# Kernel optimization log

Measured on AMD Instinct MI355X. Metric: run time of the kernel, lower is better.

The kernel has to match this reference:

```python
import jax, jax.numpy as jnp
import numpy as np

BS, C, H, W = 64, 2048, 14, 14
D = 768            # decoder_embedding
G = 100            # embed_len_decoder (groups)
F = 10             # duplicate_factor = ceil(1000/100)
NUM_CLASSES = 1000
HEADS, DH = 8, 768 # dim_head = decoder_embedding
INNER = HEADS * DH # 6144
FF = 2048          # dim_feedforward


def setup_inputs() -> dict:
    key = jax.random.key(0)
    ks = jax.random.split(key, 26)
    s = 0.02
    return {
        "x": jax.random.normal(ks[0], (BS, C, H, W), jnp.float32),
        "W_embed": jax.random.normal(ks[1], (C, D), jnp.float32) * s,
        "b_embed": jnp.zeros((D,), jnp.float32),
        "query_embed": jax.random.normal(ks[2], (G, D), jnp.float32),
        "ln1_g": jnp.ones((D,), jnp.float32), "ln1_b": jnp.zeros((D,), jnp.float32),
        "Wq_s": jax.random.normal(ks[3], (D, INNER), jnp.float32) * s,
        "Wk_s": jax.random.normal(ks[4], (D, INNER), jnp.float32) * s,
        "Wv_s": jax.random.normal(ks[5], (D, INNER), jnp.float32) * s,
        "Wo_s": jax.random.normal(ks[6], (INNER, D), jnp.float32) * s,
        "bo_s": jnp.zeros((D,), jnp.float32),
        "ln2_g": jnp.ones((D,), jnp.float32), "ln2_b": jnp.zeros((D,), jnp.float32),
        "Wq_c": jax.random.normal(ks[7], (D, INNER), jnp.float32) * s,
        "Wk_c": jax.random.normal(ks[8], (D, INNER), jnp.float32) * s,
        "Wv_c": jax.random.normal(ks[9], (D, INNER), jnp.float32) * s,
        "Wo_c": jax.random.normal(ks[10], (INNER, D), jnp.float32) * s,
        "bo_c": jnp.zeros((D,), jnp.float32),
        "ln3_g": jnp.ones((D,), jnp.float32), "ln3_b": jnp.zeros((D,), jnp.float32),
        "W1": jax.random.normal(ks[11], (D, FF), jnp.float32) * s,
        "b1": jnp.zeros((FF,), jnp.float32),
        "W2": jax.random.normal(ks[12], (FF, D), jnp.float32) * s,
        "b2": jnp.zeros((D,), jnp.float32),
        "dup_pool": jax.random.normal(ks[13], (G, D, F), jnp.float32) * s,
        "dup_bias": jnp.zeros((NUM_CLASSES,), jnp.float32),
    }


def _ln(x, g, b, eps=1e-5):
    mu = jnp.mean(x, -1, keepdims=True)
    var = jnp.mean(jnp.square(x - mu), -1, keepdims=True)
    return g * (x - mu) * jax.lax.rsqrt(var + eps) + b


def _attn(q_in, kv_in, Wq, Wk, Wv, Wo, bo):
    b, nq, _ = q_in.shape
    nk = kv_in.shape[1]
    q = (q_in @ Wq).reshape(b, nq, HEADS, DH).transpose(0, 2, 1, 3)
    k = (kv_in @ Wk).reshape(b, nk, HEADS, DH).transpose(0, 2, 1, 3)
    v = (kv_in @ Wv).reshape(b, nk, HEADS, DH).transpose(0, 2, 1, 3)
    scores = jnp.einsum("bhqd,bhkd->bhqk", q, k) * (DH ** -0.5)
    a = jax.nn.softmax(scores, axis=-1)
    o = jnp.einsum("bhqk,bhkd->bhqd", a, v).transpose(0, 2, 1, 3).reshape(b, nq, INNER)
    return o @ Wo + bo


def reference(x, W_embed, b_embed, query_embed,
              ln1_g, ln1_b, Wq_s, Wk_s, Wv_s, Wo_s, bo_s,
              ln2_g, ln2_b, Wq_c, Wk_c, Wv_c, Wo_c, bo_c,
              ln3_g, ln3_b, W1, b1, W2, b2,
              dup_pool, dup_bias):
    bs = x.shape[0]
    # [bs, C, H, W] -> [bs, H*W, C] spatial tokens
    emb = x.reshape(bs, x.shape[1], -1).transpose(0, 2, 1)
    emb = jax.nn.relu(emb @ W_embed + b_embed)          # [bs, HW, D]
    h = jnp.broadcast_to(query_embed[None], (bs, G, D))  # query tokens
    # one pre-norm decoder layer: self-attn, cross-attn, GELU MLP
    hn = _ln(h, ln1_g, ln1_b)
    h = h + _attn(hn, hn, Wq_s, Wk_s, Wv_s, Wo_s, bo_s)
    h = h + _attn(_ln(h, ln2_g, ln2_b), emb, Wq_c, Wk_c, Wv_c, Wo_c, bo_c)
    hn = _ln(h, ln3_g, ln3_b)
    h = h + (jax.nn.gelu(hn @ W1 + b1) @ W2 + b2)
    # GroupFC: per-group matmul -> single batched einsum
    out_extrap = jnp.einsum("bgd,gdf->bgf", h, dup_pool)  # [bs, G, F]
    logits = out_extrap.reshape(bs, G * F)[:, :NUM_CLASSES] + dup_bias
    return logits
```

## Files before the change

kernel.cpp:

```cpp
#include <hip/hip_runtime.h>
#include <hip/hip_bf16.h>


typedef __attribute__((ext_vector_type(8))) short short8;
typedef __attribute__((ext_vector_type(4))) short short4b;
typedef __attribute__((ext_vector_type(4))) float floatx4;

#define DEVI static __device__ __forceinline__

DEVI short f2bf(float f) {
    union { __hip_bfloat16 h; short s; } u;
    u.h = __float2bfloat16(f);
    return u.s;
}

DEVI float bf2f(short s) {
    union { float f; unsigned u; } v;
    v.u = ((unsigned)(unsigned short)s) << 16;
    return v.f;
}

DEVI void gld_lds16(const void* g, void* l) {
    __builtin_amdgcn_global_load_lds(
        (const __attribute__((address_space(1))) void*)g,
        (__attribute__((address_space(3))) void*)l, 16, 0, 0);
}

__global__ __launch_bounds__(256)
void prep_kernel(const float* __restrict__ W_embed, const float* __restrict__ W1,
                 const float* __restrict__ W2, const float* __restrict__ Wq_s,
                 const float* __restrict__ Wk_s, const float* __restrict__ Wv_s,
                 const float* __restrict__ Wo_s, const float* __restrict__ Wo_c,
                 const float* __restrict__ Wq_c, const float* __restrict__ Wk_c,
                 const float* __restrict__ Wv_c, const float* __restrict__ x,
                 const float* __restrict__ qe, const float* __restrict__ ln1_g,
                 const float* __restrict__ ln1_b,
                 short* __restrict__ WembT, short* __restrict__ W1T,
                 short* __restrict__ W2T, short* __restrict__ WqsT,
                 short* __restrict__ WksT, short* __restrict__ WvsT,
                 short* __restrict__ WosT, short* __restrict__ WoTc,
                 short* __restrict__ CQ, short* __restrict__ CK,
                 short* __restrict__ CV, short* __restrict__ xT,
                 short* __restrict__ hn1)
{
    const int bid = blockIdx.x;
    const int t = threadIdx.x;

    if (bid >= 6912 && bid < 20736) {
        int lb = bid - 6912;
        const float* in; short* out;
        if (lb < 4608)       { in = Wq_c; out = CQ; }
        else if (lb < 9216)  { in = Wk_c; out = CK; lb -= 4608; }
        else                 { in = Wv_c; out = CV; lb -= 9216; }
        const long i = (long)lb * 256 + t;
        const float4 v = ((const float4*)in)[i];
        short4b s; s[0] = f2bf(v.x); s[1] = f2bf(v.y); s[2] = f2bf(v.z); s[3] = f2bf(v.w);
        ((short4b*)out)[i] = s;
        return;
    }

    __shared__ __align__(16) short tile[64][65];

    if (bid >= 28928) {
        const int row = bid - 28928;
        float* ss  = (float*)&tile[0][0];
        float* ssq = ss + 4;
        float4 v = {0.f, 0.f, 0.f, 0.f};
        float s = 0.f, sq = 0.f;
        if (t < 192) {
            v = *(const float4*)(qe + (long)row * 768 + (t << 2));
            s  = v.x + v.y + v.z + v.w;
            sq = v.x * v.x + v.y * v.y + v.z * v.z + v.w * v.w;
            #pragma unroll
            for (int off = 32; off; off >>= 1) {
                s  += __shfl_xor(s, off);
                sq += __shfl_xor(sq, off);
            }
            if ((t & 63) == 0) { ss[t >> 6] = s; ssq[t >> 6] = sq; }
        }
        __syncthreads();
        if (t < 192) {
            s  = ss[0] + ss[1] + ss[2];
            sq = ssq[0] + ssq[1] + ssq[2];
            const float mean = s * (1.0f / 768.0f);
            const float var  = sq * (1.0f / 768.0f) - mean * mean;
            const float rstd = rsqrtf(var + 1e-5f);
            const float4 gv = *(const float4*)(ln1_g + (t << 2));
            const float4 bv = *(const float4*)(ln1_b + (t << 2));
            short4b o;
            o[0] = f2bf((v.x - mean) * rstd * gv.x + bv.x);
            o[1] = f2bf((v.y - mean) * rstd * gv.y + bv.y);
            o[2] = f2bf((v.z - mean) * rstd * gv.z + bv.z);
            o[3] = f2bf((v.w - mean) * rstd * gv.w + bv.w);
            *(short4b*)(hn1 + (long)row * 768 + (t << 2)) = o;
        }
        return;
    }

    const float* in; short* out; int R, C, ldo, bx, by;
    long ioff = 0, ooff = 0;
    if (bid < 384)       { in = W_embed; out = WembT; R = 2048; C = 768;  ldo = 2048; bx = bid % 12;  by = bid / 12; }
    else if (bid < 768)  { const int l = bid - 384;  in = W1;   out = W1T;  R = 768;  C = 2048; ldo = 768;  bx = l % 32; by = l / 32; }
    else if (bid < 1152) { const int l = bid - 768;  in = W2;   out = W2T;  R = 2048; C = 768;  ldo = 2048; bx = l % 12; by = l / 12; }
    else if (bid < 2304) { const int l = bid - 1152; in = Wq_s; out = WqsT; R = 768;  C = 6144; ldo = 768;  bx = l % 96; by = l / 96; }
    else if (bid < 3456) { const int l = bid - 2304; in = Wk_s; out = WksT; R = 768;  C = 6144; ldo = 768;  bx = l % 96; by = l / 96; }
    else if (bid < 4608) { const int l = bid - 3456; in = Wv_s; out = WvsT; R = 768;  C = 6144; ldo = 768;  bx = l % 96; by = l / 96; }
    else if (bid < 5760) { const int l = bid - 4608; in = Wo_s; out = WosT; R = 6144; C = 768;  ldo = 6144; bx = l % 12; by = l / 12; }
    else if (bid < 6912) { const int l = bid - 5760; in = Wo_c; out = WoTc; R = 6144; C = 768;  ldo = 6144; bx = l % 12; by = l / 12; }
    else {
        const int l = bid - 20736;
        const int z = l >> 7, rem = l & 127;
        in = x; out = xT; R = 2048; C = 196; ldo = 2048;
        bx = rem % 4; by = rem / 4;
        ioff = (long)z * 2048 * 196;
        ooff = (long)z * 196 * 2048;
    }

    const int bxo = bx << 6, byo = by << 6;
    const int tx = t & 63, ty = t >> 6;
    #pragma unroll
    for (int i = ty; i < 64; i += 4) {
        const int r = byo + i, c = bxo + tx;
        short v = 0;
        if (r < R && c < C) v = f2bf(in[ioff + (long)r * C + c]);
        tile[i][tx] = v;
    }
    __syncthreads();
    #pragma unroll
    for (int i = ty; i < 64; i += 4) {
        const int c = bxo + i, r = byo + tx;
        if (c < C && r < ldo) out[ooff + (long)c * ldo + r] = tile[tx][i];
    }
}

template<int ACT, bool OUT_BF16, int TBM>
__global__ __launch_bounds__(256)
void gemm_kernel(const short* __restrict__ Ap, const short* __restrict__ Bp,
                 const float* __restrict__ bias, const float* __restrict__ resid,
                 int rmod, void* __restrict__ Cp,
                 int M, int N, int K, int Mpad, int Npad,
                 int lda, int ldb, int ldc, int inner_batch,
                 long sA1, long sA2, long sB1, long sB2, long sC1, long sC2,
                 float alpha)
{
    constexpr int BK_ = 64;
    constexpr int MI  = TBM / 32;
    constexpr int ATS = TBM * BK_;
    constexpr int BTS = 128 * BK_;
    __shared__ __align__(16) short lds_all[2 * (ATS + BTS)];

    const int gx = gridDim.x, gy = gridDim.y;
    const long nwg = (long)gx * gy * gridDim.z;
    const long dfl = blockIdx.x + (long)gx * (blockIdx.y + (long)gy * blockIdx.z);
    const long qch = nwg >> 3, rch = nwg & 7;
    const long xcd = dfl & 7, idx = dfl >> 3;
    const long w = (xcd < rch ? xcd * (qch + 1) : rch * (qch + 1) + (xcd - rch) * qch) + idx;
    const int bx = (int)(w % gx);
    const long wt = w / gx;
    const int by = (int)(wt % gy);
    const int bz = (int)(wt / gy);

    const int outer = bz / inner_batch;
    const int inner = bz - outer * inner_batch;
    const long aoff = (long)outer * sA1 + (long)inner * sA2;
    const long boff = (long)outer * sB1 + (long)inner * sB2;
    const long coff = (long)outer * sC1 + (long)inner * sC2;
    const int m0 = by * TBM, n0 = bx * 128;
    const int tid = threadIdx.x;
    const int wid = tid >> 6, lane = tid & 63;
    const int wm = (wid >> 1) * (TBM / 2);
    const int wn = (wid & 1) << 6;
    const int fr = lane & 15;
    const int fk = (lane >> 4) << 3;

    const short* A = Ap + aoff;
    const short* B = Bp + boff;
    const int rowp = tid >> 3;
    const int col8 = (tid & 7) << 3;
    const int wrow = (tid >> 6) << 3;

    const bool fastA0 = (m0 + TBM <= Mpad);
    const bool fastB0 = (n0 + 128 <= Npad);

    auto stage = [&](int buf, int kt) {
        short (*As)[BK_] = reinterpret_cast<short (*)[BK_]>(lds_all + buf * (ATS + BTS));
        short (*Bs)[BK_] = reinterpret_cast<short (*)[BK_]>(lds_all + buf * (ATS + BTS) + ATS);
        if (fastA0 && (kt + BK_ <= K)) {
            const short* src = A + (long)(m0 + rowp) * lda + kt + col8;
            const long rstride = (long)lda << 5;
            #pragma unroll
            for (int p = 0; p < TBM / 32; ++p)
                gld_lds16(src + p * rstride, &As[(p << 5) + wrow][0]);
        } else {
            #pragma unroll
            for (int i = 0; i < TBM / 32; ++i) {
                const int row = rowp + (i << 5);
                const int gm = m0 + row, gk = kt + col8;
                short8 v;
                if (gm < M && gk + 8 <= K) {
                    v = *(const short8*)(A + (long)gm * lda + gk);
                } else {
                    #pragma unroll
                    for (int j = 0; j < 8; ++j)
                        v[j] = (gm < M && gk + j < K) ? A[(long)gm * lda + gk + j] : (short)0;
                }
                *(short8*)(&As[row][col8]) = v;
            }
        }
        if (fastB0 && (kt + BK_ <= K)) {
            const short* src = B + (long)(n0 + rowp) * ldb + kt + col8;
            const long rstride = (long)ldb << 5;
            #pragma unroll
            for (int p = 0; p < 4; ++p)
                gld_lds16(src + p * rstride, &Bs[(p << 5) + wrow][0]);
        } else {
            #pragma unroll
            for (int i = 0; i < 4; ++i) {
                const int row = rowp + (i << 5);
                const int gn = n0 + row, gk = kt + col8;
                short8 v;
                if (gn < N && gk + 8 <= K) {
                    v = *(const short8*)(B + (long)gn * ldb + gk);
                } else {
                    #pragma unroll
                    for (int j = 0; j < 8; ++j)
                        v[j] = (gn < N && gk + j < K) ? B[(long)gn * ldb + gk + j] : (short)0;
                }
                *(short8*)(&Bs[row][col8]) = v;
            }
        }
    };

    floatx4 acc[MI][4] = {};
    const int nk = K / BK_;

    stage(0, 0);
    __syncthreads();
    for (int t = 0; t < nk; ++t) {
        const int cur = t & 1;
        if (t + 1 < nk) stage(cur ^ 1, (t + 1) * BK_);
        const short* As = lds_all + cur * (ATS + BTS);
        const short* Bs = lds_all + cur * (ATS + BTS) + ATS;
        #pragma unroll
        for (int kk = 0; kk < BK_; kk += 32) {
            short8 af[MI], bfv[4];
            #pragma unroll
            for (int i = 0; i < MI; ++i)
                af[i] = *(const short8*)(As + (wm + (i << 4) + fr) * BK_ + kk + fk);
            #pragma unroll
            for (int j = 0; j < 4; ++j)
                bfv[j] = *(const short8*)(Bs + (wn + (j << 4) + fr) * BK_ + kk + fk);
            #pragma unroll
            for (int i = 0; i < MI; ++i)
                #pragma unroll
                for (int j = 0; j < 4; ++j)
                    acc[i][j] = __builtin_amdgcn_mfma_f32_16x16x32_bf16(af[i], bfv[j], acc[i][j], 0, 0, 0);
        }
        __syncthreads();
    }

    if constexpr (OUT_BF16) {
        short (*Cl)[128] = reinterpret_cast<short (*)[128]>(lds_all);
        #pragma unroll
        for (int j = 0; j < 4; ++j) {
            const int lcol = wn + (j << 4) + fr;
            const float bv = bias ? bias[n0 + lcol] : 0.0f;
            #pragma unroll
            for (int i = 0; i < MI; ++i) {
                #pragma unroll
                for (int r = 0; r < 4; ++r) {
                    const int lrow = wm + (i << 4) + ((lane >> 4) << 2) + r;
                    float v = acc[i][j][r] * alpha + bv;
                    if constexpr (ACT == 1) v = fmaxf(v, 0.0f);
                    if constexpr (ACT == 2) {
                        v = 0.5f * v * (1.0f + tanhf(0.7978845608028654f * (v + 0.044715f * v * v * v)));
                    }
                    if (resid)
                        v += resid[(long)((m0 + lrow) % rmod) * ldc + n0 + lcol];
                    Cl[lrow][lcol] = f2bf(v);
                }
            }
        }
        __syncthreads();
        const int pr = tid >> 4;
        const int pc = (tid & 15) << 3;
        #pragma unroll
        for (int it = 0; it < TBM / 16; ++it) {
            const int row = (it << 4) + pr;
            const int gm = m0 + row;
            if (gm < M)
                *(short8*)((short*)Cp + coff + (long)gm * ldc + n0 + pc) =
                    *(const short8*)(&Cl[row][pc]);
        }
    } else {
        #pragma unroll
        for (int j = 0; j < 4; ++j) {
            const int col = n0 + wn + (j << 4) + fr;
            if (col >= N) continue;
            const float bv = bias ? bias[col] : 0.0f;
            #pragma unroll
            for (int i = 0; i < MI; ++i) {
                #pragma unroll
                for (int r = 0; r < 4; ++r) {
                    const int row = m0 + wm + (i << 4) + ((lane >> 4) << 2) + r;
                    if (row >= M) continue;
                    float v = acc[i][j][r] * alpha + bv;
                    if constexpr (ACT == 1) v = fmaxf(v, 0.0f);
                    if constexpr (ACT == 2) {
                        v = 0.5f * v * (1.0f + tanhf(0.7978845608028654f * (v + 0.044715f * v * v * v)));
                    }
                    const long ci = coff + (long)row * ldc + col;
                    if (resid) v += resid[(long)(row % rmod) * ldc + col];
                    ((float*)Cp)[ci] = v;
                }
            }
        }
    }
}

template<int NTT, int RI>
__global__ __launch_bounds__(256)
void attn_kernel(const short* __restrict__ Qp, const short* __restrict__ Kp,
                 const short* __restrict__ VTp, short* __restrict__ Cp,
                 int nt, int nh,
                 int ldq, int ldk, int ldv, int ldc,
                 int khs, int vhs,
                 long sK, long sVT, long sC,
                 float scale)
{
    constexpr int KP   = NTT * 16;
    constexpr int PLD  = KP + 8;
    constexpr int ROWS = RI * 64;
    constexpr int KS_SH = KP * 64;
    constexpr int P_SH  = ROWS * PLD;
    constexpr int LDS_SH = (KS_SH > P_SH) ? KS_SH : P_SH;
    __shared__ __align__(16) short lds[LDS_SH];
    short (*Pl)[PLD] = reinterpret_cast<short (*)[PLD]>(lds);

    const int blk = blockIdx.x;
    const int nb = gridDim.x / nh;
    int b, h;
    if (nb == 64) {
        b = ((blk & 7) << 3) + (blk >> 6);
        h = (blk >> 3) & 7;
    } else {
        b = blk / nh; h = blk - b * nh;
    }
    const int row0 = blockIdx.z * ROWS;

    const int tid = threadIdx.x, wid = tid >> 6, lane = tid & 63;
    const int fr = lane & 15;
    const int g4 = (lane >> 4) << 2;
    const int fk = (lane >> 4) << 3;

    const short* Qh = Qp + h * 768;
    const short* Kb = Kp + (long)b * sK + h * khs;
    const short* Vb = VTp + (long)b * sVT + (long)h * vhs * ldv;

    const int wmA = wid * (RI * 16);
    floatx4 accS[RI][NTT];
    #pragma unroll
    for (int i = 0; i < RI; ++i)
        #pragma unroll
        for (int j = 0; j < NTT; ++j) accS[i][j] = (floatx4){0.f, 0.f, 0.f, 0.f};

    const short* qrow[RI];
    #pragma unroll
    for (int i = 0; i < RI; ++i)
        qrow[i] = Qh + (long)(row0 + wmA + i * 16 + fr) * ldq + fk;

    const int rowg  = (wid << 3) + (lane >> 3);
    const int slotx = ((lane & 7) ^ ((lane >> 3) & 7)) << 3;
    const short* ksrc = Kb + (long)rowg * ldk + slotx;
    short* kdst0 = lds + (wid << 9);

    for (int t = 0; t < 12; ++t) {
        const int kt = t << 6;
        #pragma unroll
        for (int p = 0; p < KP / 32; ++p)
            gld_lds16(ksrc + ((long)(p << 5) * ldk + kt), kdst0 + (p << 11));
        __syncthreads();
        #pragma unroll
        for (int kkb = 0; kkb < 2; ++kkb) {
            const int kk = kkb << 5;
            short8 aF[RI];
            #pragma unroll
            for (int i = 0; i < RI; ++i)
                aF[i] = *(const short8*)(qrow[i] + kt + kk);
            const int sl = ((((kk >> 3) + (lane >> 4)) ^ (fr & 7)) << 3);
            #pragma unroll
            for (int j = 0; j < NTT; ++j) {
                const short8 bF = *(const short8*)(lds + ((j << 4) + fr) * 64 + sl);
                #pragma unroll
                for (int i = 0; i < RI; ++i)
                    accS[i][j] = __builtin_amdgcn_mfma_f32_16x16x32_bf16(aF[i], bF, accS[i][j], 0, 0, 0);
            }
        }
        __syncthreads();
    }

    float inv[RI][4];
    #pragma unroll
    for (int i = 0; i < RI; ++i) {
        #pragma unroll
        for (int r = 0; r < 4; ++r) {
            float m = -1e30f;
            #pragma unroll
            for (int j = 0; j < NTT; ++j) {
                const int col = j * 16 + fr;
                if (col < nt) m = fmaxf(m, accS[i][j][r]);
            }
            #pragma unroll
            for (int off = 1; off < 16; off <<= 1) m = fmaxf(m, __shfl_xor(m, off));
            float s = 0.0f;
            #pragma unroll
            for (int j = 0; j < NTT; ++j) {
                const int col = j * 16 + fr;
                float e = (col < nt) ? __expf((accS[i][j][r] - m) * scale) : 0.0f;
                accS[i][j][r] = e;
                s += e;
            }
            #pragma unroll
            for (int off = 1; off < 16; off <<= 1) s += __shfl_xor(s, off);
            inv[i][r] = 1.0f / s;
        }
    }

    #pragma unroll
    for (int i = 0; i < RI; ++i)
        #pragma unroll
        for (int j = 0; j < NTT; ++j)
            #pragma unroll
            for (int r = 0; r < 4; ++r)
                Pl[wmA + i * 16 + g4 + r][j * 16 + fr] = f2bf(accS[i][j][r] * inv[i][r]);
    __syncthreads();

    constexpr int WGN = (RI == 2) ? 2 : 4;
    constexpr int NSTEP = WGN * 64;
    const int wm2 = (wid / WGN) << 6;
    const int wn2 = (wid % WGN) << 6;
    short* Cb = Cp + (long)b * sC + h * 768;

    const int chunk = 768 / gridDim.y;
    const int n0b = blockIdx.y * chunk;
    for (int n0 = n0b; n0 < n0b + chunk; n0 += NSTEP) {
        floatx4 acc2[4][4];
        #pragma unroll
        for (int i = 0; i < 4; ++i)
            #pragma unroll
            for (int j = 0; j < 4; ++j) acc2[i][j] = (floatx4){0.f, 0.f, 0.f, 0.f};
        #pragma unroll
        for (int kk = 0; kk < KP; kk += 32) {
            short8 aF[4], bF[4];
            #pragma unroll
            for (int i = 0; i < 4; ++i)
                aF[i] = *(const short8*)(&Pl[wm2 + i * 16 + fr][kk + fk]);
            #pragma unroll
            for (int j = 0; j < 4; ++j)
                bF[j] = *(const short8*)(Vb + (long)(n0 + wn2 + j * 16 + fr) * ldv + kk + fk);
            #pragma unroll
            for (int i = 0; i < 4; ++i)
                #pragma unroll
                for (int j = 0; j < 4; ++j)
                    acc2[i][j] = __builtin_amdgcn_mfma_f32_16x16x32_bf16(aF[i], bF[j], acc2[i][j], 0, 0, 0);
        }
        #pragma unroll
        for (int j = 0; j < 4; ++j) {
            const int col = n0 + wn2 + (j << 4) + fr;
            #pragma unroll
            for (int i = 0; i < 4; ++i) {
                #pragma unroll
                for (int r = 0; r < 4; ++r) {
                    const int row = row0 + wm2 + (i << 4) + g4 + r;
                    if (row < 100)
                        Cb[(long)row * ldc + col] = f2bf(acc2[i][j][r]);
                }
            }
        }
    }
}

template<int NTT>
__global__ __launch_bounds__(512)
void attn8_kernel(const short* __restrict__ Qp, const short* __restrict__ Kp,
                  const short* __restrict__ VTp, short* __restrict__ Cp,
                  int nt, int ldq, int ldk, int ldv, int ldc,
                  long sK, long sVT, long sC, float scale)
{
    constexpr int KP   = NTT * 16;
    constexpr int PLD  = KP + 8;
    constexpr int KBUF = KP * 64;
    constexpr int P_SH = 128 * PLD;
    constexpr int LDS_SH = (2 * KBUF > P_SH) ? 2 * KBUF : P_SH;
    __shared__ __align__(16) short lds[LDS_SH];
    short (*Pl)[PLD] = reinterpret_cast<short (*)[PLD]>(lds);

    const int blk = blockIdx.x;
    const int b = ((blk & 7) << 3) + (blk >> 6);
    const int h = (blk >> 3) & 7;

    const int tid = threadIdx.x, wid = tid >> 6, lane = tid & 63;
    const int fr = lane & 15;
    const int g4 = (lane >> 4) << 2;
    const int fk = (lane >> 4) << 3;

    const short* Qh = Qp + h * 768;
    const short* Kb = Kp + (long)b * sK;
    const short* Vb = VTp + (long)b * sVT;

    const int wmA = wid << 4;
    floatx4 accS[NTT];
    #pragma unroll
    for (int j = 0; j < NTT; ++j) accS[j] = (floatx4){0.f, 0.f, 0.f, 0.f};

    const short* qrow = Qh + (long)(wmA + fr) * ldq + fk;

    const int rowg  = (wid << 3) + (lane >> 3);
    const int slotx = ((lane & 7) ^ ((lane >> 3) & 7)) << 3;
    const short* ksrc = Kb + (long)rowg * ldk + slotx;

    auto stageK = [&](int buf, int kt) {
        short* dst = lds + buf * KBUF + (wid << 9);
        #pragma unroll
        for (int p = 0; p < 4; ++p)
            if (p < 3 || wid < 4)
                gld_lds16(ksrc + ((long)(p << 6) * ldk + kt), dst + (p << 12));
    };

    stageK(0, 0);
    __syncthreads();
    for (int t = 0; t < 12; ++t) {
        const int cur = t & 1;
        if (t < 11) stageK(cur ^ 1, (t + 1) << 6);
        const int kt = t << 6;
        const short* kb = lds + cur * KBUF;
        #pragma unroll
        for (int kkb = 0; kkb < 2; ++kkb) {
            const int kk = kkb << 5;
            const short8 aF = *(const short8*)(qrow + kt + kk);
            const int sl = ((((kk >> 3) + (lane >> 4)) ^ (fr & 7)) << 3);
            #pragma unroll
            for (int j = 0; j < NTT; ++j) {
                const short8 bF = *(const short8*)(kb + ((j << 4) + fr) * 64 + sl);
                accS[j] = __builtin_amdgcn_mfma_f32_16x16x32_bf16(aF, bF, accS[j], 0, 0, 0);
            }
        }
        __syncthreads();
    }

    float inv_[4];
    #pragma unroll
    for (int r = 0; r < 4; ++r) {
        float m = -1e30f;
        #pragma unroll
        for (int j = 0; j < NTT; ++j) {
            const int col = j * 16 + fr;
            if (col < nt) m = fmaxf(m, accS[j][r]);
        }
        #pragma unroll
        for (int off = 1; off < 16; off <<= 1) m = fmaxf(m, __shfl_xor(m, off));
        float s = 0.0f;
        #pragma unroll
        for (int j = 0; j < NTT; ++j) {
            const int col = j * 16 + fr;
            float e = (col < nt) ? __expf((accS[j][r] - m) * scale) : 0.0f;
            accS[j][r] = e;
            s += e;
        }
        #pragma unroll
        for (int off = 1; off < 16; off <<= 1) s += __shfl_xor(s, off);
        inv_[r] = 1.0f / s;
    }

    #pragma unroll
    for (int j = 0; j < NTT; ++j)
        #pragma unroll
        for (int r = 0; r < 4; ++r)
            Pl[wmA + g4 + r][j * 16 + fr] = f2bf(accS[j][r] * inv_[r]);
    __syncthreads();

    const int wm2 = (wid >> 2) << 6;
    const int wn2 = (wid & 3) << 6;
    short* Cb = Cp + (long)b * sC + h * 768;

    for (int n0 = 0; n0 < 768; n0 += 256) {
        #pragma unroll
        for (int jh = 0; jh < 2; ++jh) {
            floatx4 acc2[4][2];
            #pragma unroll
            for (int i = 0; i < 4; ++i)
                #pragma unroll
                for (int j = 0; j < 2; ++j) acc2[i][j] = (floatx4){0.f, 0.f, 0.f, 0.f};
            #pragma unroll
            for (int kk = 0; kk < KP; kk += 32) {
                short8 aF[4], bF[2];
                #pragma unroll
                for (int i = 0; i < 4; ++i)
                    aF[i] = *(const short8*)(&Pl[wm2 + i * 16 + fr][kk + fk]);
                #pragma unroll
                for (int j = 0; j < 2; ++j)
                    bF[j] = *(const short8*)(Vb + (long)(n0 + wn2 + (jh * 2 + j) * 16 + fr) * ldv + kk + fk);
                #pragma unroll
                for (int i = 0; i < 4; ++i)
                    #pragma unroll
                    for (int j = 0; j < 2; ++j)
                        acc2[i][j] = __builtin_amdgcn_mfma_f32_16x16x32_bf16(aF[i], bF[j], acc2[i][j], 0, 0, 0);
            }
            #pragma unroll
            for (int j = 0; j < 2; ++j) {
                const int col = n0 + wn2 + ((jh * 2 + j) << 4) + fr;
                #pragma unroll
                for (int i = 0; i < 4; ++i) {
                    #pragma unroll
                    for (int r = 0; r < 4; ++r) {
                        const int row = wm2 + (i << 4) + g4 + r;
                        if (row < 100)
                            Cb[(long)row * ldc + col] = f2bf(acc2[i][j][r]);
                    }
                }
            }
        }
    }
}

template<bool IN_F32>
__global__ __launch_bounds__(256)
void transpose_kernel(const void* __restrict__ inp, short* __restrict__ outp,
                      int R, int Cc, int ldout)
{
    __shared__ short tile[64][65];
    const long in_off = (long)blockIdx.z * R * Cc;
    const long out_off = (long)blockIdx.z * Cc * ldout;
    const int bx = blockIdx.x << 6;
    const int by = blockIdx.y << 6;
    const int tx = threadIdx.x & 63, ty = threadIdx.x >> 6;
    #pragma unroll
    for (int i = ty; i < 64; i += 4) {
        const int r = by + i, c = bx + tx;
        short v = 0;
        if (r < R && c < Cc) {
            if constexpr (IN_F32) v = f2bf(((const float*)inp)[in_off + (long)r * Cc + c]);
            else                  v = ((const short*)inp)[in_off + (long)r * Cc + c];
        }
        tile[i][tx] = v;
    }
    __syncthreads();
    #pragma unroll
    for (int i = ty; i < 64; i += 4) {
        const int c = bx + i, r = by + tx;
        if (c < Cc && r < ldout) outp[out_off + (long)c * ldout + r] = tile[tx][i];
    }
}

__global__ __launch_bounds__(192)
void ln_kernel(const float* __restrict__ x, const float* __restrict__ g,
               const float* __restrict__ b, short* __restrict__ out)
{
    const long row = blockIdx.x;
    const float* xr = x + row * 768;
    const int t = threadIdx.x;
    const float4 v = *(const float4*)(xr + (t << 2));
    float s  = v.x + v.y + v.z + v.w;
    float sq = v.x * v.x + v.y * v.y + v.z * v.z + v.w * v.w;
    #pragma unroll
    for (int off = 32; off; off >>= 1) {
        s  += __shfl_xor(s, off);
        sq += __shfl_xor(sq, off);
    }
    __shared__ float ss[4], ssq[4];
    const int w = t >> 6;
    if ((t & 63) == 0) { ss[w] = s; ssq[w] = sq; }
    __syncthreads();
    s  = ss[0] + ss[1] + ss[2];
    sq = ssq[0] + ssq[1] + ssq[2];
    const float mean = s * (1.0f / 768.0f);
    const float var  = sq * (1.0f / 768.0f) - mean * mean;
    const float rstd = rsqrtf(var + 1e-5f);
    const float4 gv = *(const float4*)(g + (t << 2));
    const float4 bv = *(const float4*)(b + (t << 2));
    short4b o;
    o[0] = f2bf((v.x - mean) * rstd * gv.x + bv.x);
    o[1] = f2bf((v.y - mean) * rstd * gv.y + bv.y);
    o[2] = f2bf((v.z - mean) * rstd * gv.z + bv.z);
    o[3] = f2bf((v.w - mean) * rstd * gv.w + bv.w);
    *(short4b*)(out + row * 768 + (t << 2)) = o;
}

template<bool DO_LN, bool PBF16>
__global__ __launch_bounds__(192)
void reduce_kernel(const void* __restrict__ part, int nsplit, long pstride,
                   const float* __restrict__ resid, int rmod,
                   const float* __restrict__ bias,
                   const float* __restrict__ g, const float* __restrict__ bvec,
                   float* __restrict__ hout, short* __restrict__ hnout)
{
    const long row = blockIdx.x;
    const int t = threadIdx.x;
    const int c = t << 2;
    const float* rr = resid + (long)(row % rmod) * 768;
    float4 v = *(const float4*)(rr + c);
    const float4 bb = *(const float4*)(bias + c);
    v.x += bb.x; v.y += bb.y; v.z += bb.z; v.w += bb.w;
    for (int s = 0; s < nsplit; ++s) {
        const long idx = (long)s * pstride + row * 768 + c;
        if constexpr (PBF16) {
            const short4b p = *(const short4b*)((const short*)part + idx);
            v.x += bf2f(p[0]); v.y += bf2f(p[1]); v.z += bf2f(p[2]); v.w += bf2f(p[3]);
        } else {
            const float4 p = *(const float4*)((const float*)part + idx);
            v.x += p.x; v.y += p.y; v.z += p.z; v.w += p.w;
        }
    }
    *(float4*)(hout + row * 768 + c) = v;
    if constexpr (DO_LN) {
        float s  = v.x + v.y + v.z + v.w;
        float sq = v.x * v.x + v.y * v.y + v.z * v.z + v.w * v.w;
        #pragma unroll
        for (int off = 32; off; off >>= 1) {
            s  += __shfl_xor(s, off);
            sq += __shfl_xor(sq, off);
        }
        __shared__ float ss[4], ssq[4];
        const int wv = t >> 6;
        if ((t & 63) == 0) { ss[wv] = s; ssq[wv] = sq; }
        __syncthreads();
        s  = ss[0] + ss[1] + ss[2];
        sq = ssq[0] + ssq[1] + ssq[2];
        const float mean = s * (1.0f / 768.0f);
        const float var  = sq * (1.0f / 768.0f) - mean * mean;
        const float rstd = rsqrtf(var + 1e-5f);
        const float4 gv = *(const float4*)(g + c);
        const float4 bv = *(const float4*)(bvec + c);
        short4b o;
        o[0] = f2bf((v.x - mean) * rstd * gv.x + bv.x);
        o[1] = f2bf((v.y - mean) * rstd * gv.y + bv.y);
        o[2] = f2bf((v.z - mean) * rstd * gv.z + bv.z);
        o[3] = f2bf((v.w - mean) * rstd * gv.w + bv.w);
        *(short4b*)(hnout + row * 768 + c) = o;
    }
}

__global__ __launch_bounds__(192)
void reducen_kernel(const short* __restrict__ part, int nsplit, long pstride,
                    short* __restrict__ out, int grps)
{
    const int blk = blockIdx.x;
    const int row = blk / grps, grp = blk - row * grps;
    const long base = (long)row * grps * 768 + grp * 768 + (threadIdx.x << 2);
    float4 v = {0.f, 0.f, 0.f, 0.f};
    for (int s = 0; s < nsplit; ++s) {
        const short4b p = *(const short4b*)(part + (long)s * pstride + base);
        v.x += bf2f(p[0]); v.y += bf2f(p[1]); v.z += bf2f(p[2]); v.w += bf2f(p[3]);
    }
    short4b o;
    o[0] = f2bf(v.x); o[1] = f2bf(v.y); o[2] = f2bf(v.z); o[3] = f2bf(v.w);
    *(short4b*)(out + base) = o;
}

__global__ __launch_bounds__(64)
void groupfc_kernel(const float* __restrict__ h, const float* __restrict__ dp,
                    const float* __restrict__ bias, float* __restrict__ out)
{
    const int bg = blockIdx.x;
    const int g = bg % 100;
    const int t = threadIdx.x;
    const float* hr = h + (long)bg * 768;
    const float* d = dp + (long)g * 7680;
    float acc[10];
    #pragma unroll
    for (int f = 0; f < 10; ++f) acc[f] = 0.0f;
    for (int k = t; k < 768; k += 64) {
        const float hv = hr[k];
        const float* dr = d + k * 10;
        #pragma unroll
        for (int f = 0; f < 10; ++f) acc[f] += hv * dr[f];
    }
    #pragma unroll
    for (int f = 0; f < 10; ++f) {
        #pragma unroll
        for (int off = 32; off; off >>= 1) acc[f] += __shfl_xor(acc[f], off);
    }
    if (t == 0) {
        const int b = bg / 100;
        #pragma unroll
        for (int f = 0; f < 10; ++f)
            out[(long)b * 1000 + g * 10 + f] = acc[f] + bias[g * 10 + f];
    }
}

extern "C" void kernel_launch(void* const* d_in, const int* in_sizes, int n_in,
                              void* d_out, int out_size, void* d_ws, size_t ws_size,
                              hipStream_t stream)
{
    const float* x       = (const float*)d_in[0];
    const float* W_embed = (const float*)d_in[1];
    const float* b_embed = (const float*)d_in[2];
    const float* qe      = (const float*)d_in[3];
    const float* ln1_g   = (const float*)d_in[4];
    const float* ln1_b   = (const float*)d_in[5];
    const float* Wq_s    = (const float*)d_in[6];
    const float* Wk_s    = (const float*)d_in[7];
    const float* Wv_s    = (const float*)d_in[8];
    const float* Wo_s    = (const float*)d_in[9];
    const float* bo_s    = (const float*)d_in[10];
    const float* ln2_g   = (const float*)d_in[11];
    const float* ln2_b   = (const float*)d_in[12];
    const float* Wq_c    = (const float*)d_in[13];
    const float* Wk_c    = (const float*)d_in[14];
    const float* Wv_c    = (const float*)d_in[15];
    const float* Wo_c    = (const float*)d_in[16];
    const float* bo_c    = (const float*)d_in[17];
    const float* ln3_g   = (const float*)d_in[18];
    const float* ln3_b   = (const float*)d_in[19];
    const float* W1      = (const float*)d_in[20];
    const float* b1      = (const float*)d_in[21];
    const float* W2      = (const float*)d_in[22];
    const float* b2      = (const float*)d_in[23];
    const float* dpool   = (const float*)d_in[24];
    const float* dbias   = (const float*)d_in[25];

    char* base = (char*)d_ws;
    size_t off = 0;
    auto alloc = [&](size_t bytes) -> void* {
        void* p = base + off;
        off += (bytes + 255) & ~(size_t)255;
        return p;
    };
    short* ek    = (short*)alloc(12544L * 768 * 2);
    short* ekT   = (short*)alloc(64L * 768 * 256 * 2);
    short* big   = (short*)alloc(6400L * 6144 * 2);
    char*  shr   = (char*) alloc(4L * 6400 * 768 * 4);
    float* h2    = (float*)alloc(6400L * 768 * 4);
    short* hn3   = (short*)alloc(6400L * 768 * 2);
    short* t1    = (short*)alloc(6400L * 2048 * 2);
    short* WembT = (short*)alloc(768L * 2048 * 2);
    short* W1T   = (short*)alloc(2048L * 768 * 2);
    short* W2T   = (short*)alloc(768L * 2048 * 2);
    short* WqkTc = (short*)alloc(6144L * 768 * 2);
    short* WvoTc = (short*)alloc(768L * 6144 * 2);
    short* WqsT  = (short*)alloc(6144L * 768 * 2);
    short* WksT  = (short*)alloc(6144L * 768 * 2);
    short* WvsT  = (short*)alloc(6144L * 768 * 2);
    short* WosT  = (short*)alloc(768L * 6144 * 2);
    short* hn1   = (short*)alloc(128L * 768 * 2);
    short* q_s   = (short*)alloc(128L * 6144 * 2);
    short* k_s   = (short*)alloc(128L * 6144 * 2);
    short* v_s   = (short*)alloc(128L * 6144 * 2);
    short* ctx_s = (short*)alloc(128L * 6144 * 2);
    short* v_sT  = (short*)alloc(6144L * 128 * 2);
    short* qt_c  = (short*)alloc(128L * 6144 * 2);
    short* qtP   = (short*)alloc(4L * 100 * 6144 * 2);
    float* partS = (float*)alloc(8L * 100 * 768 * 4);
    float* h1    = (float*)alloc(128L * 768 * 4);
    short* hn2   = (short*)alloc(128L * 768 * 2);
    (void)ws_size; (void)in_sizes; (void)n_in; (void)out_size;

    short* CQ    = (short*)shr;
    short* CK    = CQ + 4718592L;
    short* CV    = CK + 4718592L;
    short* WoTc  = CV + 4718592L;
    short* partCb = (short*)shr;

    const float scale = 0.03608439182435161f;

    short* xT = big;
    prep_kernel<<<dim3(29028), 256, 0, stream>>>(
        W_embed, W1, W2, Wq_s, Wk_s, Wv_s, Wo_s, Wo_c,
        Wq_c, Wk_c, Wv_c, x, qe, ln1_g, ln1_b,
        WembT, W1T, W2T, WqsT, WksT, WvsT, WosT, WoTc,
        CQ, CK, CV, xT, hn1);

    gemm_kernel<0, true, 128><<<dim3(6, 6, 8), 256, 0, stream>>>(
        CK, CQ, nullptr, nullptr, 1, WqkTc,
        768, 768, 768, 768, 768, 6144, 6144, 768, 8,
        0L, 768L, 0L, 768L, 0L, 589824L, 1.0f);
    gemm_kernel<0, true, 128><<<dim3(6, 6, 8), 256, 0, stream>>>(
        WoTc, CV, nullptr, nullptr, 1, WvoTc,
        768, 768, 768, 768, 768, 6144, 6144, 6144, 8,
        0L, 768L, 0L, 768L, 0L, 768L, 1.0f);

    gemm_kernel<1, true, 64><<<dim3(6, 196, 1), 256, 0, stream>>>(
        xT, WembT, b_embed, nullptr, 1, ek,
        12544, 768, 2048, 12544, 768, 2048, 2048, 768, 1,
        0L, 0L, 0L, 0L, 0L, 0L, 1.0f);
    transpose_kernel<false><<<dim3(12, 4, 64), 256, 0, stream>>>(ek, ekT, 196, 768, 256);

    gemm_kernel<0, true, 128><<<dim3(48, 1, 3), 256, 0, stream>>>(
        hn1, WqsT, nullptr, nullptr, 1, q_s,
        100, 6144, 768, 128, 6144, 768, 768, 6144, 1,
        0L, 0L, 4718592L, 0L, 786432L, 0L, 1.0f);
    transpose_kernel<false><<<dim3(96, 2, 1), 256, 0, stream>>>(v_s, v_sT, 100, 6144, 128);
    attn_kernel<8, 2><<<dim3(8, 6, 1), 256, 0, stream>>>(
        q_s, k_s, v_sT, ctx_s,
        100, 8, 6144, 6144, 128, 6144,
        768, 768, 0L, 0L, 0L, scale);
    gemm_kernel<0, false, 128><<<dim3(6, 1, 8), 256, 0, stream>>>(
        ctx_s, WosT, nullptr, nullptr, 1, partS,
        100, 768, 768, 128, 768, 6144, 6144, 768, 8,
        0L, 768L, 0L, 768L, 0L, 76800L, 1.0f);
    reduce_kernel<true, false><<<dim3(100), 192, 0, stream>>>(
        partS, 8, 76800L, qe, 100, bo_s, ln2_g, ln2_b, h1, hn2);

    gemm_kernel<0, true, 128><<<dim3(48, 1, 4), 256, 0, stream>>>(
        hn2, WqkTc, nullptr, nullptr, 1, qtP,
        100, 6144, 192, 128, 6144, 768, 768, 6144, 4,
        0L, 192L, 0L, 192L, 0L, 614400L, 1.0f);
    reducen_kernel<<<dim3(800), 192, 0, stream>>>(qtP, 4, 614400L, qt_c, 8);
    attn8_kernel<14><<<dim3(512), 512, 0, stream>>>(
        qt_c, ek, ekT, big,
        196, 6144, 768, 256, 6144,
        150528L, 196608L, 614400L, scale);
    gemm_kernel<0, true, 128><<<dim3(6, 50, 8), 256, 0, stream>>>(
        big, WvoTc, nullptr, nullptr, 1, partCb,
        6400, 768, 768, 6400, 768, 6144, 6144, 768, 8,
        0L, 768L, 0L, 768L, 0L, 4915200L, 1.0f);
    reduce_kernel<true, true><<<dim3(6400), 192, 0, stream>>>(
        partCb, 8, 4915200L, h1, 100, bo_c, ln3_g, ln3_b, h2, hn3);

    gemm_kernel<2, true, 64><<<dim3(16, 100, 1), 256, 0, stream>>>(
        hn3, W1T, b1, nullptr, 1, t1,
        6400, 2048, 768, 6400, 2048, 768, 768, 2048, 1, 0,0,0,0,0,0, 1.0f);
    gemm_kernel<0, true, 128><<<dim3(6, 50, 4), 256, 0, stream>>>(
        t1, W2T, nullptr, nullptr, 1, partCb,
        6400, 768, 512, 6400, 768, 2048, 2048, 768, 4,
        0L, 512L, 0L, 512L, 0L, 4915200L, 1.0f);
    reduce_kernel<false, true><<<dim3(6400), 192, 0, stream>>>(
        partCb, 4, 4915200L, h2, 6400, b2, nullptr, nullptr, h2, nullptr);

    groupfc_kernel<<<dim3(6400), 64, 0, stream>>>(h2, dpool, dbias, (float*)d_out);
}
```

Before: 752.2 us.

## Fuse fp32-to-bf16 weight conversion into GEMM operand loads, drop prep passes

Removes the separate prep passes that converted and transposed the self-attention weights and the cross-attention Q/K/V weights into bf16 scratch copies. The GEMMs now read fp32 weights directly and convert them to bf16 while staging into LDS. A new B mode transposes row-major weights into padded LDS, and an A mode does the same conversion for fp32 A operands. This saves the extra global write and re-read of about 100MB of weight copies. In exchange, the converting loads skip the direct global-to-LDS path and read fp32, which doubles the bytes loaded per GEMM tile, and the transposed LDS stores are scalar and may cause bank conflicts.

```diff
diff --git a/kernel.cpp b/kernel.cpp
--- a/kernel.cpp
+++ b/kernel.cpp
@@ -28,41 +28,21 @@
 
 __global__ __launch_bounds__(256)
 void prep_kernel(const float* __restrict__ W_embed, const float* __restrict__ W1,
-                 const float* __restrict__ W2, const float* __restrict__ Wq_s,
-                 const float* __restrict__ Wk_s, const float* __restrict__ Wv_s,
-                 const float* __restrict__ Wo_s, const float* __restrict__ Wo_c,
-                 const float* __restrict__ Wq_c, const float* __restrict__ Wk_c,
-                 const float* __restrict__ Wv_c, const float* __restrict__ x,
+                 const float* __restrict__ W2, const float* __restrict__ Wo_c,
+                 const float* __restrict__ x,
                  const float* __restrict__ qe, const float* __restrict__ ln1_g,
                  const float* __restrict__ ln1_b,
                  short* __restrict__ WembT, short* __restrict__ W1T,
-                 short* __restrict__ W2T, short* __restrict__ WqsT,
-                 short* __restrict__ WksT, short* __restrict__ WvsT,
-                 short* __restrict__ WosT, short* __restrict__ WoTc,
-                 short* __restrict__ CQ, short* __restrict__ CK,
-                 short* __restrict__ CV, short* __restrict__ xT,
-                 short* __restrict__ hn1)
+                 short* __restrict__ W2T, short* __restrict__ WoTc,
+                 short* __restrict__ xT, short* __restrict__ hn1)
 {
     const int bid = blockIdx.x;
     const int t = threadIdx.x;
 
-    if (bid >= 6912 && bid < 20736) {
-        int lb = bid - 6912;
-        const float* in; short* out;
-        if (lb < 4608)       { in = Wq_c; out = CQ; }
-        else if (lb < 9216)  { in = Wk_c; out = CK; lb -= 4608; }
-        else                 { in = Wv_c; out = CV; lb -= 9216; }
-        const long i = (long)lb * 256 + t;
-        const float4 v = ((const float4*)in)[i];
-        short4b s; s[0] = f2bf(v.x); s[1] = f2bf(v.y); s[2] = f2bf(v.z); s[3] = f2bf(v.w);
-        ((short4b*)out)[i] = s;
-        return;
-    }
-
     __shared__ __align__(16) short tile[64][65];
 
-    if (bid >= 28928) {
-        const int row = bid - 28928;
+    if (bid >= 10496) {
+        const int row = bid - 10496;
         float* ss  = (float*)&tile[0][0];
         float* ssq = ss + 4;
         float4 v = {0.f, 0.f, 0.f, 0.f};
@@ -102,13 +82,9 @@
     if (bid < 384)       { in = W_embed; out = WembT; R = 2048; C = 768;  ldo = 2048; bx = bid % 12;  by = bid / 12; }
     else if (bid < 768)  { const int l = bid - 384;  in = W1;   out = W1T;  R = 768;  C = 2048; ldo = 768;  bx = l % 32; by = l / 32; }
     else if (bid < 1152) { const int l = bid - 768;  in = W2;   out = W2T;  R = 2048; C = 768;  ldo = 2048; bx = l % 12; by = l / 12; }
-    else if (bid < 2304) { const int l = bid - 1152; in = Wq_s; out = WqsT; R = 768;  C = 6144; ldo = 768;  bx = l % 96; by = l / 96; }
-    else if (bid < 3456) { const int l = bid - 2304; in = Wk_s; out = WksT; R = 768;  C = 6144; ldo = 768;  bx = l % 96; by = l / 96; }
-    else if (bid < 4608) { const int l = bid - 3456; in = Wv_s; out = WvsT; R = 768;  C = 6144; ldo = 768;  bx = l % 96; by = l / 96; }
-    else if (bid < 5760) { const int l = bid - 4608; in = Wo_s; out = WosT; R = 6144; C = 768;  ldo = 6144; bx = l % 12; by = l / 12; }
-    else if (bid < 6912) { const int l = bid - 5760; in = Wo_c; out = WoTc; R = 6144; C = 768;  ldo = 6144; bx = l % 12; by = l / 12; }
+    else if (bid < 2304) { const int l = bid - 1152; in = Wo_c; out = WoTc; R = 6144; C = 768;  ldo = 6144; bx = l % 12; by = l / 12; }
     else {
-        const int l = bid - 20736;
+        const int l = bid - 2304;
         const int z = l >> 7, rem = l & 127;
         in = x; out = xT; R = 2048; C = 196; ldo = 2048;
         bx = rem % 4; by = rem / 4;
@@ -133,9 +109,9 @@
     }
 }
 
-template<int ACT, bool OUT_BF16, int TBM>
+template<int ACT, bool OUT_BF16, int TBM, int AM = 0, int BMODE = 0>
 __global__ __launch_bounds__(256)
-void gemm_kernel(const short* __restrict__ Ap, const short* __restrict__ Bp,
+void gemm_kernel(const void* __restrict__ Ap, const void* __restrict__ Bp,
                  const float* __restrict__ bias, const float* __restrict__ resid,
                  int rmod, void* __restrict__ Cp,
                  int M, int N, int K, int Mpad, int Npad,
@@ -145,8 +121,9 @@
 {
     constexpr int BK_ = 64;
     constexpr int MI  = TBM / 32;
+    constexpr int BLD = (BMODE == 2) ? 66 : 64;
     constexpr int ATS = TBM * BK_;
-    constexpr int BTS = 128 * BK_;
+    constexpr int BTS = 128 * BLD;
     __shared__ __align__(16) short lds_all[2 * (ATS + BTS)];
 
     const int gx = gridDim.x, gy = gridDim.y;
@@ -173,8 +150,6 @@
     const int fr = lane & 15;
     const int fk = (lane >> 4) << 3;
 
-    const short* A = Ap + aoff;
-    const short* B = Bp + boff;
     const int rowp = tid >> 3;
     const int col8 = (tid & 7) << 3;
     const int wrow = (tid >> 6) << 3;
@@ -183,50 +158,92 @@
     const bool fastB0 = (n0 + 128 <= Npad);
 
     auto stage = [&](int buf, int kt) {
-        short (*As)[BK_] = reinterpret_cast<short (*)[BK_]>(lds_all + buf * (ATS + BTS));
-        short (*Bs)[BK_] = reinterpret_cast<short (*)[BK_]>(lds_all + buf * (ATS + BTS) + ATS);
-        if (fastA0 && (kt + BK_ <= K)) {
-            const short* src = A + (long)(m0 + rowp) * lda + kt + col8;
-            const long rstride = (long)lda << 5;
-            #pragma unroll
-            for (int p = 0; p < TBM / 32; ++p)
-                gld_lds16(src + p * rstride, &As[(p << 5) + wrow][0]);
+        short* As = lds_all + buf * (ATS + BTS);
+        short* Bs = As + ATS;
+        if constexpr (AM == 0) {
+            const short* A = (const short*)Ap + aoff;
+            if (fastA0 && (kt + BK_ <= K)) {
+                const short* src = A + (long)(m0 + rowp) * lda + kt + col8;
+                const long rstride = (long)lda << 5;
+                #pragma unroll
+                for (int p = 0; p < TBM / 32; ++p)
+                    gld_lds16(src + p * rstride, As + ((p << 5) + wrow) * BK_);
+            } else {
+                #pragma unroll
+                for (int i = 0; i < TBM / 32; ++i) {
+                    const int row = rowp + (i << 5);
+                    const int gm = m0 + row, gk = kt + col8;
+                    short8 v;
+                    if (gm < M && gk + 8 <= K) {
+                        v = *(const short8*)(A + (long)gm * lda + gk);
+                    } else {
+                        #pragma unroll
+                        for (int j = 0; j < 8; ++j)
+                            v[j] = (gm < M && gk + j < K) ? A[(long)gm * lda + gk + j] : (short)0;
+                    }
+                    *(short8*)(As + row * BK_ + col8) = v;
+                }
+            }
         } else {
-            #pragma unroll
-            for (int i = 0; i < TBM / 32; ++i) {
-                const int row = rowp + (i << 5);
-                const int gm = m0 + row, gk = kt + col8;
-                short8 v;
-                if (gm < M && gk + 8 <= K) {
-                    v = *(const short8*)(A + (long)gm * lda + gk);
-                } else {
-                    #pragma unroll
-                    for (int j = 0; j < 8; ++j)
-                        v[j] = (gm < M && gk + j < K) ? A[(long)gm * lda + gk + j] : (short)0;
+            const float* A = (const float*)Ap + aoff;
+            const int r0 = tid >> 4, c4 = (tid & 15) << 2;
+            #pragma unroll
+            for (int i = 0; i < TBM / 16; ++i) {
+                const int row = r0 + (i << 4);
+                const int gm = m0 + row, gk = kt + c4;
+                float4 v = {0.f, 0.f, 0.f, 0.f};
+                if (gm < M) v = *(const float4*)(A + (long)gm * lda + gk);
+                short4b s; s[0] = f2bf(v.x); s[1] = f2bf(v.y); s[2] = f2bf(v.z); s[3] = f2bf(v.w);
+                *(short4b*)(As + row * BK_ + c4) = s;
+            }
+        }
+        if constexpr (BMODE == 0) {
+            const short* B = (const short*)Bp + boff;
+            if (fastB0 && (kt + BK_ <= K)) {
+                const short* src = B + (long)(n0 + rowp) * ldb + kt + col8;
+                const long rstride = (long)ldb << 5;
+                #pragma unroll
+                for (int p = 0; p < 4; ++p)
+                    gld_lds16(src + p * rstride, Bs + ((p << 5) + wrow) * BLD);
+            } else {
+                #pragma unroll
+                for (int i = 0; i < 4; ++i) {
+                    const int row = rowp + (i << 5);
+                    const int gn = n0 + row, gk = kt + col8;
+                    short8 v;
+                    if (gn < N && gk + 8 <= K) {
+                        v = *(const short8*)(B + (long)gn * ldb + gk);
+                    } else {
+                        #pragma unroll
+                        for (int j = 0; j < 8; ++j)
+                            v[j] = (gn < N && gk + j < K) ? B[(long)gn * ldb + gk + j] : (short)0;
+                    }
+                    *(short8*)(Bs + row * BLD + col8) = v;
                 }
-                *(short8*)(&As[row][col8]) = v;
-            }
-        }
-        if (fastB0 && (kt + BK_ <= K)) {
-            const short* src = B + (long)(n0 + rowp) * ldb + kt + col8;
-            const long rstride = (long)ldb << 5;
-            #pragma unroll
-            for (int p = 0; p < 4; ++p)
-                gld_lds16(src + p * rstride, &Bs[(p << 5) + wrow][0]);
+            }
+        } else if constexpr (BMODE == 1) {
+            const float* B = (const float*)Bp + boff;
+            const int r0 = tid >> 4, c4 = (tid & 15) << 2;
+            #pragma unroll
+            for (int i = 0; i < 8; ++i) {
+                const int row = r0 + (i << 4);
+                const int gn = n0 + row, gk = kt + c4;
+                float4 v = {0.f, 0.f, 0.f, 0.f};
+                if (gn < N) v = *(const float4*)(B + (long)gn * ldb + gk);
+                short4b s; s[0] = f2bf(v.x); s[1] = f2bf(v.y); s[2] = f2bf(v.z); s[3] = f2bf(v.w);
+                *(short4b*)(Bs + row * BLD + c4) = s;
+            }
         } else {
-            #pragma unroll
-            for (int i = 0; i < 4; ++i) {
-                const int row = rowp + (i << 5);
-                const int gn = n0 + row, gk = kt + col8;
-                short8 v;
-                if (gn < N && gk + 8 <= K) {
-                    v = *(const short8*)(B + (long)gn * ldb + gk);
-                } else {
-                    #pragma unroll
-                    for (int j = 0; j < 8; ++j)
-                        v[j] = (gn < N && gk + j < K) ? B[(long)gn * ldb + gk + j] : (short)0;
-                }
-                *(short8*)(&Bs[row][col8]) = v;
+            const float* B = (const float*)Bp + boff;
+            const int kr = tid >> 5, nc = (tid & 31) << 2;
+            #pragma unroll
+            for (int i = 0; i < 8; ++i) {
+                const int k = kr + (i << 3);
+                const float4 v = *(const float4*)(B + (long)(kt + k) * ldb + n0 + nc);
+                Bs[(nc + 0) * BLD + k] = f2bf(v.x);
+                Bs[(nc + 1) * BLD + k] = f2bf(v.y);
+                Bs[(nc + 2) * BLD + k] = f2bf(v.z);
+                Bs[(nc + 3) * BLD + k] = f2bf(v.w);
             }
         }
     };
@@ -240,7 +257,7 @@
         const int cur = t & 1;
         if (t + 1 < nk) stage(cur ^ 1, (t + 1) * BK_);
         const short* As = lds_all + cur * (ATS + BTS);
-        const short* Bs = lds_all + cur * (ATS + BTS) + ATS;
+        const short* Bs = As + ATS;
         #pragma unroll
         for (int kk = 0; kk < BK_; kk += 32) {
             short8 af[MI], bfv[4];
@@ -249,7 +266,7 @@
                 af[i] = *(const short8*)(As + (wm + (i << 4) + fr) * BK_ + kk + fk);
             #pragma unroll
             for (int j = 0; j < 4; ++j)
-                bfv[j] = *(const short8*)(Bs + (wn + (j << 4) + fr) * BK_ + kk + fk);
+                bfv[j] = *(const short8*)(Bs + (wn + (j << 4) + fr) * BLD + kk + fk);
             #pragma unroll
             for (int i = 0; i < MI; ++i)
                 #pragma unroll
@@ -650,40 +667,6 @@
         const int c = bx + i, r = by + tx;
         if (c < Cc && r < ldout) outp[out_off + (long)c * ldout + r] = tile[tx][i];
     }
-}
-
-__global__ __launch_bounds__(192)
-void ln_kernel(const float* __restrict__ x, const float* __restrict__ g,
-               const float* __restrict__ b, short* __restrict__ out)
-{
-    const long row = blockIdx.x;
-    const float* xr = x + row * 768;
-    const int t = threadIdx.x;
-    const float4 v = *(const float4*)(xr + (t << 2));
-    float s  = v.x + v.y + v.z + v.w;
-    float sq = v.x * v.x + v.y * v.y + v.z * v.z + v.w * v.w;
-    #pragma unroll
-    for (int off = 32; off; off >>= 1) {
-        s  += __shfl_xor(s, off);
-        sq += __shfl_xor(sq, off);
-    }
-    __shared__ float ss[4], ssq[4];
-    const int w = t >> 6;
-    if ((t & 63) == 0) { ss[w] = s; ssq[w] = sq; }
-    __syncthreads();
-    s  = ss[0] + ss[1] + ss[2];
-    sq = ssq[0] + ssq[1] + ssq[2];
-    const float mean = s * (1.0f / 768.0f);
-    const float var  = sq * (1.0f / 768.0f) - mean * mean;
-    const float rstd = rsqrtf(var + 1e-5f);
-    const float4 gv = *(const float4*)(g + (t << 2));
-    const float4 bv = *(const float4*)(b + (t << 2));
-    short4b o;
-    o[0] = f2bf((v.x - mean) * rstd * gv.x + bv.x);
-    o[1] = f2bf((v.y - mean) * rstd * gv.y + bv.y);
-    o[2] = f2bf((v.z - mean) * rstd * gv.z + bv.z);
-    o[3] = f2bf((v.w - mean) * rstd * gv.w + bv.w);
-    *(short4b*)(out + row * 768 + (t << 2)) = o;
 }
 
 template<bool DO_LN, bool PBF16>
@@ -838,10 +821,7 @@
     short* W2T   = (short*)alloc(768L * 2048 * 2);
     short* WqkTc = (short*)alloc(6144L * 768 * 2);
     short* WvoTc = (short*)alloc(768L * 6144 * 2);
-    short* WqsT  = (short*)alloc(6144L * 768 * 2);
-    short* WksT  = (short*)alloc(6144L * 768 * 2);
-    short* WvsT  = (short*)alloc(6144L * 768 * 2);
-    short* WosT  = (short*)alloc(768L * 6144 * 2);
+    short* WoTc  = (short*)alloc(768L * 6144 * 2);
     short* hn1   = (short*)alloc(128L * 768 * 2);
     short* q_s   = (short*)alloc(128L * 6144 * 2);
     short* k_s   = (short*)alloc(128L * 6144 * 2);
@@ -855,27 +835,21 @@
     short* hn2   = (short*)alloc(128L * 768 * 2);
     (void)ws_size; (void)in_sizes; (void)n_in; (void)out_size;
 
-    short* CQ    = (short*)shr;
-    short* CK    = CQ + 4718592L;
-    short* CV    = CK + 4718592L;
-    short* WoTc  = CV + 4718592L;
     short* partCb = (short*)shr;
 
     const float scale = 0.03608439182435161f;
 
     short* xT = big;
-    prep_kernel<<<dim3(29028), 256, 0, stream>>>(
-        W_embed, W1, W2, Wq_s, Wk_s, Wv_s, Wo_s, Wo_c,
-        Wq_c, Wk_c, Wv_c, x, qe, ln1_g, ln1_b,
-        WembT, W1T, W2T, WqsT, WksT, WvsT, WosT, WoTc,
-        CQ, CK, CV, xT, hn1);
-
-    gemm_kernel<0, true, 128><<<dim3(6, 6, 8), 256, 0, stream>>>(
-        CK, CQ, nullptr, nullptr, 1, WqkTc,
+    prep_kernel<<<dim3(10596), 256, 0, stream>>>(
+        W_embed, W1, W2, Wo_c, x, qe, ln1_g, ln1_b,
+        WembT, W1T, W2T, WoTc, xT, hn1);
+
+    gemm_kernel<0, true, 128, 1, 1><<<dim3(6, 6, 8), 256, 0, stream>>>(
+        Wk_c, Wq_c, nullptr, nullptr, 1, WqkTc,
         768, 768, 768, 768, 768, 6144, 6144, 768, 8,
         0L, 768L, 0L, 768L, 0L, 589824L, 1.0f);
-    gemm_kernel<0, true, 128><<<dim3(6, 6, 8), 256, 0, stream>>>(
-        WoTc, CV, nullptr, nullptr, 1, WvoTc,
+    gemm_kernel<0, true, 128, 0, 1><<<dim3(6, 6, 8), 256, 0, stream>>>(
+        WoTc, Wv_c, nullptr, nullptr, 1, WvoTc,
         768, 768, 768, 768, 768, 6144, 6144, 6144, 8,
         0L, 768L, 0L, 768L, 0L, 768L, 1.0f);
 
@@ -885,19 +859,24 @@
         0L, 0L, 0L, 0L, 0L, 0L, 1.0f);
     transpose_kernel<false><<<dim3(12, 4, 64), 256, 0, stream>>>(ek, ekT, 196, 768, 256);
 
-    gemm_kernel<0, true, 128><<<dim3(48, 1, 3), 256, 0, stream>>>(
-        hn1, WqsT, nullptr, nullptr, 1, q_s,
-        100, 6144, 768, 128, 6144, 768, 768, 6144, 1,
-        0L, 0L, 4718592L, 0L, 786432L, 0L, 1.0f);
+    gemm_kernel<0, true, 128, 0, 2><<<dim3(48, 1, 1), 256, 0, stream>>>(
+        hn1, Wq_s, nullptr, nullptr, 1, q_s,
+        100, 6144, 768, 128, 6144, 768, 6144, 6144, 1, 0,0,0,0,0,0, 1.0f);
+    gemm_kernel<0, true, 128, 0, 2><<<dim3(48, 1, 1), 256, 0, stream>>>(
+        hn1, Wk_s, nullptr, nullptr, 1, k_s,
+        100, 6144, 768, 128, 6144, 768, 6144, 6144, 1, 0,0,0,0,0,0, 1.0f);
+    gemm_kernel<0, true, 128, 0, 2><<<dim3(48, 1, 1), 256, 0, stream>>>(
+        hn1, Wv_s, nullptr, nullptr, 1, v_s,
+        100, 6144, 768, 128, 6144, 768, 6144, 6144, 1, 0,0,0,0,0,0, 1.0f);
     transpose_kernel<false><<<dim3(96, 2, 1), 256, 0, stream>>>(v_s, v_sT, 100, 6144, 128);
     attn_kernel<8, 2><<<dim3(8, 6, 1), 256, 0, stream>>>(
         q_s, k_s, v_sT, ctx_s,
         100, 8, 6144, 6144, 128, 6144,
         768, 768, 0L, 0L, 0L, scale);
-    gemm_kernel<0, false, 128><<<dim3(6, 1, 8), 256, 0, stream>>>(
-        ctx_s, WosT, nullptr, nullptr, 1, partS,
-        100, 768, 768, 128, 768, 6144, 6144, 768, 8,
-        0L, 768L, 0L, 768L, 0L, 76800L, 1.0f);
+    gemm_kernel<0, false, 128, 0, 2><<<dim3(6, 1, 8), 256, 0, stream>>>(
+        ctx_s, Wo_s, nullptr, nullptr, 1, partS,
+        100, 768, 768, 128, 768, 6144, 768, 768, 8,
+        0L, 768L, 0L, 589824L, 0L, 76800L, 1.0f);
     reduce_kernel<true, false><<<dim3(100), 192, 0, stream>>>(
         partS, 8, 76800L, qe, 100, bo_s, ln2_g, ln2_b, h1, hn2);
 
```

Result: slower. 1.076 ms (+43.1%).
